# Optimization experiments

Measured on AMD Instinct MI355X. Metric: run time of the kernel, lower is better.

Reference implementation:

```python
import jax, jax.numpy as jnp
import numpy as np

BSZ, D = 256, 512
LOGIT_SCALE = 1.0


def setup_inputs() -> dict:
    key = jax.random.key(0)
    k1, k2, k3 = jax.random.split(key, 3)
    x = jax.random.normal(k1, (BSZ, D), dtype=jnp.float32)
    y = jax.random.normal(k2, (BSZ, D), dtype=jnp.float32)
    z = jax.random.normal(k3, (BSZ, D), dtype=jnp.float32)
    return {"x": x, "y": y, "z": z}


def _logits_n_squared(anchor, a, b, shift):
    # torch recursion: products[i*bsz + r] = a[r] * roll(b, i)[r] = a[r] * b[(r - i) % bsz]
    bsz = anchor.shape[0]
    P = a[None, :, :] * b[shift]              # (i, r, d) = (bsz, bsz, d)
    logits = jnp.einsum('ad,ird->air', anchor, P)  # (a, i, r)
    return LOGIT_SCALE * logits.reshape(bsz, bsz * bsz)


def _cross_entropy_diag(logits):
    bsz = logits.shape[0]
    lp = jax.nn.log_softmax(logits, axis=-1)
    idx = jnp.arange(bsz)
    return -jnp.mean(lp[idx, idx])


def reference(x, y, z):
    bsz = x.shape[0]
    r = jnp.arange(bsz)
    shift = (r[None, :] - r[:, None]) % bsz   # (i, r): index into b after roll by i
    reps = [x, y, z]
    losses = []
    for i in range(3):
        anchor = reps[i]
        non_anchor = [reps[j] for j in range(3) if j != i]
        logits = _logits_n_squared(anchor, non_anchor[0], non_anchor[1], shift)
        losses.append(_cross_entropy_diag(logits))
    return sum(losses) / 3.0
```

## Files before the change

### kernel.cpp

```cpp
#include <hip/hip_runtime.h>

#define DIM 512
#define ASTRIDE 40

typedef unsigned int uint;
typedef unsigned short ushort;
typedef __attribute__((ext_vector_type(8))) short short8;
typedef __attribute__((ext_vector_type(4))) float f32x4;

#define GLOAD_LDS(g, l) __builtin_amdgcn_global_load_lds( \
    (const __attribute__((address_space(1))) void*)(g), \
    (__attribute__((address_space(3))) void*)(l), 16, 0, 0)

__device__ __forceinline__ uint pack_bf16(float a, float b) {
    union { float f; uint u; } ua, ub;
    ua.f = a; ub.f = b;
    uint x0 = ua.u + 0x8000u;
    uint x1 = ub.u + 0x8000u;
    return __builtin_amdgcn_perm(x1, x0, 0x07060302);
}

__global__ void zconv_kernel(const float* __restrict__ z, ushort* __restrict__ zb) {
    int t = blockIdx.x * 256 + threadIdx.x;
    int f = t * 4;
    float4 a = *(const float4*)(z + f);
    uint2 o;
    o.x = pack_bf16(a.x, a.y);
    o.y = pack_bf16(a.z, a.w);
    *(uint2*)(zb + f) = o;
}

__global__ void __launch_bounds__(512, 4)
gemm_fused(const float* __restrict__ x, const float* __restrict__ y,
           const ushort* __restrict__ zb, const float* __restrict__ z,
           float* __restrict__ rowM, float* __restrict__ rowS,
           float* __restrict__ colM, float* __restrict__ colS,
           float* __restrict__ diag, uint* __restrict__ counter) {
    __shared__ __align__(16) float xs[DIM];
    __shared__ __align__(16) ushort As[2][128 * ASTRIDE];
    __shared__ __align__(16) ushort Bs[3][256 * 32];
    __shared__ float redA[128 * 4];
    __shared__ float rowMaxS[128];
    __shared__ float redB[256 * 2];
    __shared__ float colMaxS[256];
    __shared__ float dred[8];

    const int tid = threadIdx.x;
    const int a   = blockIdx.x >> 1;
    const int rt  = blockIdx.x & 1;

    if (blockIdx.x == 0 && tid == 0) *counter = 0u;

    xs[tid] = x[a * DIM + tid];

    const int lane = tid & 63;
    const int wave = tid >> 6;
    const int quad = lane >> 4;
    const int ln15 = lane & 15;
    const int wr = wave >> 2;
    const int wc = wave & 3;

    if (rt == 0) {
        float p = xs[tid] * y[a * DIM + tid] * z[a * DIM + tid];
        #pragma unroll
        for (int m = 1; m < 64; m <<= 1) p += __shfl_xor(p, m, 64);
        if (lane == 0) dred[wave] = p;
        __syncthreads();
        if (tid == 0) {
            float s = 0.f;
            #pragma unroll
            for (int w2 = 0; w2 < 8; ++w2) s += dred[w2];
            diag[a] = s;
        }
    }
    __syncthreads();

    f32x4 acc[4][4];
    #pragma unroll
    for (int i = 0; i < 4; ++i)
        #pragma unroll
        for (int j = 0; j < 4; ++j)
            acc[i][j] = (f32x4){0.f, 0.f, 0.f, 0.f};

    const int rA = tid >> 2;
    const int kA = (tid & 3) * 8;
    const float* yrow = y + (rt * 128 + rA) * DIM + kA;

    const int s0 = wave * 128 + lane;
    const int row0 = s0 >> 2, kc0 = ((s0 & 3) - (row0 >> 1)) & 3;
    const ushort* gB0 = zb + row0 * DIM + kc0 * 8;
    const int s1 = s0 + 64;
    const int row1 = s1 >> 2, kc1 = ((s1 & 3) - (row1 >> 1)) & 3;
    const ushort* gB1 = zb + row1 * DIM + kc1 * 8;

    float4 ya = *(const float4*)(yrow);
    float4 yb = *(const float4*)(yrow + 4);
    __builtin_amdgcn_sched_barrier(0);
    GLOAD_LDS(gB0, &Bs[0][wave * 1024]);
    GLOAD_LDS(gB1, &Bs[0][wave * 1024 + 512]);
    GLOAD_LDS(gB0 + 32, &Bs[1][wave * 1024]);
    GLOAD_LDS(gB1 + 32, &Bs[1][wave * 1024 + 512]);
    {
        float4 x0 = *(const float4*)(xs + kA);
        float4 x1 = *(const float4*)(xs + kA + 4);
        uint4 o;
        o.x = pack_bf16(ya.x * x0.x, ya.y * x0.y);
        o.y = pack_bf16(ya.z * x0.z, ya.w * x0.w);
        o.z = pack_bf16(yb.x * x1.x, yb.y * x1.y);
        o.w = pack_bf16(yb.z * x1.z, yb.w * x1.w);
        *(uint4*)(&As[0][rA * ASTRIDE + kA]) = o;
    }
    asm volatile("s_waitcnt vmcnt(2) lgkmcnt(0)" ::: "memory");
    __builtin_amdgcn_s_barrier();
    __builtin_amdgcn_sched_barrier(0);

    int biCur = 0, biN2 = 2;
    for (int kt = 0; kt < 16; ++kt) {
        if (kt < 15) {
            ya = *(const float4*)(yrow + (kt + 1) * 32);
            yb = *(const float4*)(yrow + (kt + 1) * 32 + 4);
        }
        __builtin_amdgcn_sched_barrier(0);
        if (kt < 14) {
            GLOAD_LDS(gB0 + (kt + 2) * 32, &Bs[biN2][wave * 1024]);
            GLOAD_LDS(gB1 + (kt + 2) * 32, &Bs[biN2][wave * 1024 + 512]);
        }
        short8 af[4], bfr[4];
        #pragma unroll
        for (int i = 0; i < 4; ++i)
            af[i] = *(const short8*)(&As[kt & 1][(wr * 64 + i * 16 + ln15) * ASTRIDE + quad * 8]);
        #pragma unroll
        for (int j = 0; j < 4; ++j) {
            int row = wc * 64 + j * 16 + ln15;
            int pos = row * 4 + ((quad + (row >> 1)) & 3);
            bfr[j] = *(const short8*)(&Bs[biCur][pos * 8]);
        }
        #pragma unroll
        for (int i = 0; i < 4; ++i)
            #pragma unroll
            for (int j = 0; j < 4; ++j)
                acc[i][j] = __builtin_amdgcn_mfma_f32_16x16x32_bf16(af[i], bfr[j], acc[i][j], 0, 0, 0);
        if (kt < 15) {
            const int k1 = (kt + 1) * 32;
            float4 x0 = *(const float4*)(xs + k1 + kA);
            float4 x1 = *(const float4*)(xs + k1 + kA + 4);
            uint4 o;
            o.x = pack_bf16(ya.x * x0.x, ya.y * x0.y);
            o.y = pack_bf16(ya.z * x0.z, ya.w * x0.w);
            o.z = pack_bf16(yb.x * x1.x, yb.y * x1.y);
            o.w = pack_bf16(yb.z * x1.z, yb.w * x1.w);
            *(uint4*)(&As[(kt + 1) & 1][rA * ASTRIDE + kA]) = o;
        }
        asm volatile("s_waitcnt vmcnt(2) lgkmcnt(0)" ::: "memory");
        __builtin_amdgcn_s_barrier();
        __builtin_amdgcn_sched_barrier(0);
        int tmp = biCur; biCur = biCur + 1 == 3 ? 0 : biCur + 1;
        biN2 = biN2 + 1 == 3 ? 0 : biN2 + 1; (void)tmp;
    }
    __syncthreads();

    #pragma unroll
    for (int i = 0; i < 4; ++i) {
        #pragma unroll
        for (int reg = 0; reg < 4; ++reg) {
            float m = fmaxf(fmaxf(acc[i][0][reg], acc[i][1][reg]),
                            fmaxf(acc[i][2][reg], acc[i][3][reg]));
            #pragma unroll
            for (int d = 1; d < 16; d <<= 1) m = fmaxf(m, __shfl_xor(m, d, 64));
            if (ln15 == 0) redA[(wr * 64 + i * 16 + quad * 4 + reg) * 4 + wc] = m;
        }
    }
    __syncthreads();
    if (tid < 128) {
        float m = fmaxf(fmaxf(redA[tid * 4 + 0], redA[tid * 4 + 1]),
                        fmaxf(redA[tid * 4 + 2], redA[tid * 4 + 3]));
        rowMaxS[tid] = m;
    }
    __syncthreads();
    #pragma unroll
    for (int i = 0; i < 4; ++i) {
        #pragma unroll
        for (int reg = 0; reg < 4; ++reg) {
            int r = wr * 64 + i * 16 + quad * 4 + reg;
            float rm = rowMaxS[r];
            float s = __expf(acc[i][0][reg] - rm) + __expf(acc[i][1][reg] - rm)
                    + __expf(acc[i][2][reg] - rm) + __expf(acc[i][3][reg] - rm);
            #pragma unroll
            for (int d = 1; d < 16; d <<= 1) s += __shfl_xor(s, d, 64);
            if (ln15 == 0) redA[r * 4 + wc] = s;
        }
    }
    __syncthreads();
    if (tid < 128) {
        float s = redA[tid * 4 + 0] + redA[tid * 4 + 1] + redA[tid * 4 + 2] + redA[tid * 4 + 3];
        int rg = rt * 128 + tid;
        rowM[a * 256 + rg] = rowMaxS[tid];
        rowS[a * 256 + rg] = s;
    }

    #pragma unroll
    for (int j = 0; j < 4; ++j) {
        float m = -3.4e38f;
        #pragma unroll
        for (int i = 0; i < 4; ++i)
            #pragma unroll
            for (int reg = 0; reg < 4; ++reg)
                m = fmaxf(m, acc[i][j][reg]);
        m = fmaxf(m, __shfl_xor(m, 16, 64));
        m = fmaxf(m, __shfl_xor(m, 32, 64));
        if (quad == 0) redB[(wc * 64 + j * 16 + ln15) * 2 + wr] = m;
    }
    __syncthreads();
    if (tid < 256) colMaxS[tid] = fmaxf(redB[tid * 2], redB[tid * 2 + 1]);
    __syncthreads();
    #pragma unroll
    for (int j = 0; j < 4; ++j) {
        int n = wc * 64 + j * 16 + ln15;
        float cm = colMaxS[n];
        float s = 0.f;
        #pragma unroll
        for (int i = 0; i < 4; ++i)
            #pragma unroll
            for (int reg = 0; reg < 4; ++reg)
                s += __expf(acc[i][j][reg] - cm);
        s += __shfl_xor(s, 16, 64);
        s += __shfl_xor(s, 32, 64);
        if (quad == 0) redB[n * 2 + wr] = s;
    }
    __syncthreads();
    if (tid < 256) {
        float s = redB[tid * 2] + redB[tid * 2 + 1];
        colM[(a * 256 + tid) * 2 + rt] = colMaxS[tid];
        colS[(a * 256 + tid) * 2 + rt] = s;
    }
}

__device__ __forceinline__ float blk_max(float v, float* sm) {
    #pragma unroll
    for (int d = 1; d < 64; d <<= 1) v = fmaxf(v, __shfl_xor(v, d, 64));
    __syncthreads();
    if ((threadIdx.x & 63) == 0) sm[threadIdx.x >> 6] = v;
    __syncthreads();
    return fmaxf(fmaxf(sm[0], sm[1]), fmaxf(sm[2], sm[3]));
}
__device__ __forceinline__ float blk_sum(float v, float* sm) {
    #pragma unroll
    for (int d = 1; d < 64; d <<= 1) v += __shfl_xor(v, d, 64);
    __syncthreads();
    if ((threadIdx.x & 63) == 0) sm[threadIdx.x >> 6] = v;
    __syncthreads();
    return sm[0] + sm[1] + sm[2] + sm[3];
}

__global__ void combine_final(const float* __restrict__ rowM, const float* __restrict__ rowS,
                              const float* __restrict__ colM, const float* __restrict__ colS,
                              const float* __restrict__ diag,
                              float* __restrict__ m123, uint* __restrict__ counter,
                              float* __restrict__ out) {
    __shared__ float sm[4];
    __shared__ uint isLast;
    int b = blockIdx.x, t = threadIdx.x;
    float m = rowM[b * 256 + t], s = rowS[b * 256 + t];
    float M = blk_max(m, sm);
    float S = blk_sum(s * __expf(m - M), sm);
    float M1 = M + __logf(S);
    m = rowM[t * 256 + b]; s = rowS[t * 256 + b];
    M = blk_max(m, sm);
    S = blk_sum(s * __expf(m - M), sm);
    float M2 = M + __logf(S);
    float am = colM[(t * 256 + b) * 2 + 0], av = colS[(t * 256 + b) * 2 + 0];
    float bm = colM[(t * 256 + b) * 2 + 1], bv = colS[(t * 256 + b) * 2 + 1];
    m = fmaxf(am, bm);
    s = av * __expf(am - m) + bv * __expf(bm - m);
    M = blk_max(m, sm);
    S = blk_sum(s * __expf(m - M), sm);
    float M3 = M + __logf(S);
    if (t == 0) {
        m123[b] = M1 + M2 + M3;
        __threadfence();
        isLast = (atomicAdd(counter, 1u) == 255u) ? 1u : 0u;
    }
    __syncthreads();
    if (isLast) {
        __threadfence();
        const volatile float* vm = (const volatile float*)m123;
        const volatile float* vd = (const volatile float*)diag;
        float S1 = blk_sum(vm[t], sm);
        float S2 = blk_sum(vd[t], sm);
        if (t == 0) out[0] = S1 / 768.0f - S2 / 256.0f;
    }
}

extern "C" void kernel_launch(void* const* d_in, const int* in_sizes, int n_in,
                              void* d_out, int out_size, void* d_ws, size_t ws_size,
                              hipStream_t stream) {
    const float* x = (const float*)d_in[0];
    const float* y = (const float*)d_in[1];
    const float* z = (const float*)d_in[2];
    char* w = (char*)d_ws;
    ushort* zb  = (ushort*)(w);
    float* rowM = (float*)(w + 262144);
    float* rowS = (float*)(w + 524288);
    float* colM = (float*)(w + 786432);
    float* colS = (float*)(w + 1310720);
    float* diag = (float*)(w + 1835008);
    float* m123 = (float*)(w + 1836032);
    uint*  counter = (uint*)(w + 1837056);
    float* out  = (float*)d_out;

    zconv_kernel<<<128, 256, 0, stream>>>(z, zb);
    gemm_fused<<<512, 512, 0, stream>>>(x, y, zb, z, rowM, rowS, colM, colS, diag, counter);
    combine_final<<<256, 256, 0, stream>>>(rowM, rowS, colM, colS, diag, m123, counter, out);
}
```

Measured before the change: 98.75 us.

## Double-buffer B tiles and interleave A-tile packing between MFMA groups

Cuts the B-tile LDS ring from three buffers to two, prefetching only one k-step ahead, and unrolls the k loop by two so buffer indices become compile-time constants. The next A tile is packed between the two halves of the MFMA block so its VALU work overlaps matrix math. Waits now drain all outstanding loads (vmcnt(0)) each step. This saves LDS, which may raise occupancy, and removes index bookkeeping, at the cost of less load lookahead and more exposed global-load latency per iteration.

```diff
diff --git a/kernel.cpp b/kernel.cpp
--- a/kernel.cpp
+++ b/kernel.cpp
@@ -38,7 +38,7 @@
            float* __restrict__ diag, uint* __restrict__ counter) {
     __shared__ __align__(16) float xs[DIM];
     __shared__ __align__(16) ushort As[2][128 * ASTRIDE];
-    __shared__ __align__(16) ushort Bs[3][256 * 32];
+    __shared__ __align__(16) ushort Bs[2][256 * 32];
     __shared__ float redA[128 * 4];
     __shared__ float rowMaxS[128];
     __shared__ float redB[256 * 2];
@@ -98,8 +98,6 @@
     __builtin_amdgcn_sched_barrier(0);
     GLOAD_LDS(gB0, &Bs[0][wave * 1024]);
     GLOAD_LDS(gB1, &Bs[0][wave * 1024 + 512]);
-    GLOAD_LDS(gB0 + 32, &Bs[1][wave * 1024]);
-    GLOAD_LDS(gB1 + 32, &Bs[1][wave * 1024 + 512]);
     {
         float4 x0 = *(const float4*)(xs + kA);
         float4 x1 = *(const float4*)(xs + kA + 4);
@@ -110,53 +108,66 @@
         o.w = pack_bf16(yb.z * x1.z, yb.w * x1.w);
         *(uint4*)(&As[0][rA * ASTRIDE + kA]) = o;
     }
-    asm volatile("s_waitcnt vmcnt(2) lgkmcnt(0)" ::: "memory");
+    asm volatile("s_waitcnt vmcnt(0) lgkmcnt(0)" ::: "memory");
     __builtin_amdgcn_s_barrier();
     __builtin_amdgcn_sched_barrier(0);
 
-    int biCur = 0, biN2 = 2;
-    for (int kt = 0; kt < 16; ++kt) {
-        if (kt < 15) {
-            ya = *(const float4*)(yrow + (kt + 1) * 32);
-            yb = *(const float4*)(yrow + (kt + 1) * 32 + 4);
-        }
-        __builtin_amdgcn_sched_barrier(0);
-        if (kt < 14) {
-            GLOAD_LDS(gB0 + (kt + 2) * 32, &Bs[biN2][wave * 1024]);
-            GLOAD_LDS(gB1 + (kt + 2) * 32, &Bs[biN2][wave * 1024 + 512]);
-        }
-        short8 af[4], bfr[4];
-        #pragma unroll
-        for (int i = 0; i < 4; ++i)
-            af[i] = *(const short8*)(&As[kt & 1][(wr * 64 + i * 16 + ln15) * ASTRIDE + quad * 8]);
-        #pragma unroll
-        for (int j = 0; j < 4; ++j) {
-            int row = wc * 64 + j * 16 + ln15;
-            int pos = row * 4 + ((quad + (row >> 1)) & 3);
-            bfr[j] = *(const short8*)(&Bs[biCur][pos * 8]);
-        }
-        #pragma unroll
-        for (int i = 0; i < 4; ++i)
-            #pragma unroll
-            for (int j = 0; j < 4; ++j)
-                acc[i][j] = __builtin_amdgcn_mfma_f32_16x16x32_bf16(af[i], bfr[j], acc[i][j], 0, 0, 0);
-        if (kt < 15) {
-            const int k1 = (kt + 1) * 32;
-            float4 x0 = *(const float4*)(xs + k1 + kA);
-            float4 x1 = *(const float4*)(xs + k1 + kA + 4);
-            uint4 o;
-            o.x = pack_bf16(ya.x * x0.x, ya.y * x0.y);
-            o.y = pack_bf16(ya.z * x0.z, ya.w * x0.w);
-            o.z = pack_bf16(yb.x * x1.x, yb.y * x1.y);
-            o.w = pack_bf16(yb.z * x1.z, yb.w * x1.w);
-            *(uint4*)(&As[(kt + 1) & 1][rA * ASTRIDE + kA]) = o;
-        }
-        asm volatile("s_waitcnt vmcnt(2) lgkmcnt(0)" ::: "memory");
-        __builtin_amdgcn_s_barrier();
-        __builtin_amdgcn_sched_barrier(0);
-        int tmp = biCur; biCur = biCur + 1 == 3 ? 0 : biCur + 1;
-        biN2 = biN2 + 1 == 3 ? 0 : biN2 + 1; (void)tmp;
-    }
+#define KT_PHASE(KT, CUR, NXT)                                                  \
+    {                                                                           \
+        if ((KT) < 15) {          \
+            ya = *(const float4*)(yrow + ((KT) + 1) * 32);                      \
+            yb = *(const float4*)(yrow + ((KT) + 1) * 32 + 4);                  \
+        }                                                                       \
+        __builtin_amdgcn_sched_barrier(0);                                      \
+        if ((KT) < 15) {                   \
+            GLOAD_LDS(gB0 + ((KT) + 1) * 32, &Bs[NXT][wave * 1024]);            \
+            GLOAD_LDS(gB1 + ((KT) + 1) * 32, &Bs[NXT][wave * 1024 + 512]);      \
+        }                                                                       \
+        short8 af0, af1, af2, af3, bfr[4];                                      \
+        _Pragma("unroll")                                                       \
+        for (int j = 0; j < 4; ++j) {                                           \
+            int row = wc * 64 + j * 16 + ln15;                                  \
+            int pos = row * 4 + ((quad + (row >> 1)) & 3);                      \
+            bfr[j] = *(const short8*)(&Bs[CUR][pos * 8]);                       \
+        }                                                                       \
+        af0 = *(const short8*)(&As[CUR][(wr * 64 +  0 + ln15) * ASTRIDE + quad * 8]); \
+        af1 = *(const short8*)(&As[CUR][(wr * 64 + 16 + ln15) * ASTRIDE + quad * 8]); \
+        af2 = *(const short8*)(&As[CUR][(wr * 64 + 32 + ln15) * ASTRIDE + quad * 8]); \
+        af3 = *(const short8*)(&As[CUR][(wr * 64 + 48 + ln15) * ASTRIDE + quad * 8]); \
+        _Pragma("unroll")                                                       \
+        for (int j = 0; j < 4; ++j)                                             \
+            acc[0][j] = __builtin_amdgcn_mfma_f32_16x16x32_bf16(af0, bfr[j], acc[0][j], 0, 0, 0); \
+        _Pragma("unroll")                                                       \
+        for (int j = 0; j < 4; ++j)                                             \
+            acc[1][j] = __builtin_amdgcn_mfma_f32_16x16x32_bf16(af1, bfr[j], acc[1][j], 0, 0, 0); \
+        if ((KT) < 15) {    \
+            const int k1 = ((KT) + 1) * 32;                                     \
+            float4 x0 = *(const float4*)(xs + k1 + kA);                         \
+            float4 x1 = *(const float4*)(xs + k1 + kA + 4);                     \
+            uint4 o;                                                            \
+            o.x = pack_bf16(ya.x * x0.x, ya.y * x0.y);                          \
+            o.y = pack_bf16(ya.z * x0.z, ya.w * x0.w);                          \
+            o.z = pack_bf16(yb.x * x1.x, yb.y * x1.y);                          \
+            o.w = pack_bf16(yb.z * x1.z, yb.w * x1.w);                          \
+            *(uint4*)(&As[NXT][rA * ASTRIDE + kA]) = o;                         \
+        }                                                                       \
+        _Pragma("unroll")                                                       \
+        for (int j = 0; j < 4; ++j)                                             \
+            acc[2][j] = __builtin_amdgcn_mfma_f32_16x16x32_bf16(af2, bfr[j], acc[2][j], 0, 0, 0); \
+        _Pragma("unroll")                                                       \
+        for (int j = 0; j < 4; ++j)                                             \
+            acc[3][j] = __builtin_amdgcn_mfma_f32_16x16x32_bf16(af3, bfr[j], acc[3][j], 0, 0, 0); \
+        asm volatile("s_waitcnt vmcnt(0) lgkmcnt(0)" ::: "memory");             \
+        __builtin_amdgcn_s_barrier();                                           \
+        __builtin_amdgcn_sched_barrier(0);                                      \
+    }
+
+    for (int kt2 = 0; kt2 < 8; ++kt2) {
+        const int ktE = kt2 * 2;
+        KT_PHASE(ktE,     0, 1);
+        KT_PHASE(ktE + 1, 1, 0);
+    }
+#undef KT_PHASE
     __syncthreads();
 
     #pragma unroll
```

New measurement: 100.3 us. Within noise of the previous version (+1.5%).
